# Kernel optimization log

Measured on AMD Instinct MI355X. Metric: run time of the kernel, lower is better.

Reference implementation:

```python
import jax, jax.numpy as jnp
import numpy as np

N = 1024    # num_points
HID = 1024  # Hamiltonian MLP hidden width


def setup_inputs() -> dict:
    key = jax.random.key(0)
    ks = jax.random.split(key, 6)
    def w(k, shape, fan_in):
        return jax.random.normal(k, shape, dtype=jnp.float32) / np.float32(np.sqrt(fan_in))
    return {
        "x": jax.random.normal(ks[0], (N,), dtype=jnp.float32),
        "q": jax.random.normal(ks[1], (N,), dtype=jnp.float32),
        "p": jax.random.normal(ks[2], (N,), dtype=jnp.float32),
        "W1": w(ks[3], (3 * N, HID), 3 * N),
        "b1": jnp.zeros((HID,), dtype=jnp.float32),
        "W2": w(ks[4], (HID, HID), HID),
        "b2": jnp.zeros((HID,), dtype=jnp.float32),
        "W3": w(ks[5], (HID, 1), HID),
        "b3": jnp.zeros((1,), dtype=jnp.float32),
    }


def _hamiltonian(z, W1, b1, W2, b2, W3, b3):
    # H: R^{3N} -> scalar (matches self.H(cat([x,q,p])).sum())
    h = jnp.tanh(z @ W1 + b1)
    h = jnp.tanh(h @ W2 + b2)
    return jnp.sum(h @ W3 + b3)


def reference(x, q, p, W1, b1, W2, b2, W3, b3):
    n = x.shape[0]

    def grads_qp(x_):
        # (dH/dq, dH/dp) as a function of x, with q,p closed over
        f = lambda q_, p_: _hamiltonian(jnp.concatenate([x_, q_, p_]), W1, b1, W2, b2, W3, b3)
        return jax.grad(f, argnums=(0, 1))(q, p)  # each [n]

    # Diagonal of cross-Hessian blocks via forward-over-reverse, batched over
    # all n basis directions at once (replaces the per-index autograd loop).
    eye = jnp.eye(n, dtype=x.dtype)

    def diag_entry(e_i, i):
        _, (dgq, dgp) = jax.jvp(grads_qp, (x,), (e_i,))
        return dgq[i], dgp[i]  # d2H/(dx_i dq_i), d2H/(dx_i dp_i)

    dH_dq_dx, dH_dp_dx = jax.vmap(diag_entry)(eye, jnp.arange(n))  # each [n]
    return dH_dp_dx, -dH_dq_dx
```

## Files before the change

kernel.cpp:

```cpp
#include <hip/hip_runtime.h>
#include <math.h>

typedef unsigned short u16;
typedef __bf16 bf16x8 __attribute__((ext_vector_type(8)));
typedef float f32x4 __attribute__((ext_vector_type(4)));

__device__ inline u16 bf16_rn(float x) {
    unsigned u = __float_as_uint(x);
    return (u16)((u + 0x7FFFu + ((u >> 16) & 1u)) >> 16);
}
__device__ inline void split2(float x, u16& h, u16& l) {
    h = bf16_rn(x);
    float hf = __uint_as_float(((unsigned)h) << 16);
    l = bf16_rn(x - hf);
}
__device__ inline uint2 pack4(u16 a, u16 b, u16 c, u16 d) {
    uint2 r;
    r.x = (unsigned)a | ((unsigned)b << 16);
    r.y = (unsigned)c | ((unsigned)d << 16);
    return r;
}
__device__ inline f32x4 mfma16(bf16x8 a, bf16x8 b, f32x4 c) {
    return __builtin_amdgcn_mfma_f32_16x16x32_bf16(a, b, c, 0, 0, 0);
}

__global__ __launch_bounds__(256) void k_pre(const float* __restrict__ x,
                                             const float* __restrict__ q,
                                             const float* __restrict__ p,
                                             const float* __restrict__ W1,
                                             u16* __restrict__ Ah, u16* __restrict__ Al,
                                             float* __restrict__ Upart,
                                             float* __restrict__ out,
                                             float* __restrict__ Vacc) {
    int b = blockIdx.x, t = threadIdx.x;
    if (b < 1024) {
        int idx = (b * 256 + t) * 4;
        float4 v = *(const float4*)(W1 + idx);
        u16 h0, l0, h1, l1, h2, l2, h3, l3;
        split2(v.x, h0, l0); split2(v.y, h1, l1); split2(v.z, h2, l2); split2(v.w, h3, l3);
        *(uint2*)&Ah[idx] = pack4(h0, h1, h2, h3);
        *(uint2*)&Al[idx] = pack4(l0, l1, l2, l3);
    } else if (b < 1216) {
        int jc = b - 1024;
        int k = (jc & 3) * 256 + t;
        int j0 = (jc >> 2) * 64;
        __shared__ float zs[64];
        if (t < 64) {
            int j = j0 + t;
            zs[t] = (j < 1024) ? x[j] : (j < 2048 ? q[j - 1024] : p[j - 2048]);
        }
        __syncthreads();
        float acc = 0.f;
#pragma unroll 8
        for (int j = 0; j < 64; ++j) acc += zs[j] * W1[(j0 + j) * 1024 + k];
        Upart[(jc >> 2) * 1024 + k] = acc;
    } else {
        int idx = ((b - 1216) * 256 + t) * 4;
        if (idx < 2048) *(float4*)(out + idx) = make_float4(0.f, 0.f, 0.f, 0.f);
        else *(float4*)(Vacc + idx - 2048) = make_float4(0.f, 0.f, 0.f, 0.f);
    }
}

__global__ __launch_bounds__(256) void k_w2v(const float* __restrict__ W2,
                                             const float* __restrict__ b1,
                                             const float* __restrict__ Upart,
                                             float* __restrict__ H1g, float* __restrict__ D1g,
                                             u16* __restrict__ W2h, u16* __restrict__ W2l,
                                             u16* __restrict__ WTh, u16* __restrict__ WTl,
                                             float* __restrict__ Vacc) {
    __shared__ float T[64][65];
    __shared__ float hs[64], ds[64];
    int k0 = blockIdx.y * 64, m0 = blockIdx.x * 64;
    int t = threadIdx.x;
    if (t < 64) {
        float u = 0.f;
#pragma unroll 8
        for (int c = 0; c < 48; ++c) u += Upart[c * 1024 + k0 + t];
        float h = tanhf(u + b1[k0 + t]);
        hs[t] = h;
        ds[t] = 1.f - h * h;
        if (m0 == 0) { H1g[k0 + t] = h; D1g[k0 + t] = 1.f - h * h; }
    }
    __syncthreads();
    int rr = t >> 4, cc = (t & 15) * 4;
    float4 vp = make_float4(0.f, 0.f, 0.f, 0.f);
#pragma unroll
    for (int j = 0; j < 4; ++j) {
        int r = rr + j * 16;
        float4 v = *(const float4*)(W2 + (k0 + r) * 1024 + m0 + cc);
        T[r][cc + 0] = v.x; T[r][cc + 1] = v.y; T[r][cc + 2] = v.z; T[r][cc + 3] = v.w;
        u16 h0, l0, h1, l1, h2, l2, h3, l3;
        split2(v.x, h0, l0); split2(v.y, h1, l1); split2(v.z, h2, l2); split2(v.w, h3, l3);
        *(uint2*)&W2h[(k0 + r) * 1024 + m0 + cc] = pack4(h0, h1, h2, h3);
        *(uint2*)&W2l[(k0 + r) * 1024 + m0 + cc] = pack4(l0, l1, l2, l3);
        float hk = hs[r];
        vp.x += hk * v.x; vp.y += hk * v.y; vp.z += hk * v.z; vp.w += hk * v.w;
    }
    vp.x += __shfl_xor(vp.x, 16); vp.y += __shfl_xor(vp.y, 16);
    vp.z += __shfl_xor(vp.z, 16); vp.w += __shfl_xor(vp.w, 16);
    vp.x += __shfl_xor(vp.x, 32); vp.y += __shfl_xor(vp.y, 32);
    vp.z += __shfl_xor(vp.z, 32); vp.w += __shfl_xor(vp.w, 32);
    if (((t & 63) >> 4) == 0) {
        atomicAdd(&Vacc[m0 + cc + 0], vp.x);
        atomicAdd(&Vacc[m0 + cc + 1], vp.y);
        atomicAdd(&Vacc[m0 + cc + 2], vp.z);
        atomicAdd(&Vacc[m0 + cc + 3], vp.w);
    }
    __syncthreads();
#pragma unroll
    for (int j = 0; j < 4; ++j) {
        int mrow = rr + j * 16;
        float f0 = T[cc + 0][mrow] * ds[cc + 0];
        float f1 = T[cc + 1][mrow] * ds[cc + 1];
        float f2 = T[cc + 2][mrow] * ds[cc + 2];
        float f3 = T[cc + 3][mrow] * ds[cc + 3];
        u16 h0, l0, h1, l1, h2, l2, h3, l3;
        split2(f0, h0, l0); split2(f1, h1, l1); split2(f2, h2, l2); split2(f3, h3, l3);
        *(uint2*)&WTh[(m0 + mrow) * 1024 + k0 + cc] = pack4(h0, h1, h2, h3);
        *(uint2*)&WTl[(m0 + mrow) * 1024 + k0 + cc] = pack4(l0, l1, l2, l3);
    }
}

__global__ __launch_bounds__(256) void k_g(const float* __restrict__ W2,
                                           const float* __restrict__ Vacc,
                                           const float* __restrict__ b2,
                                           const float* __restrict__ W3,
                                           const float* __restrict__ H1,
                                           const float* __restrict__ D1,
                                           float* __restrict__ Avec) {
    __shared__ float sv[1024];
    int k = blockIdx.x;
    int t = threadIdx.x;
#pragma unroll
    for (int j = 0; j < 4; ++j) {
        int m = t * 4 + j;
        float h = tanhf(Vacc[m] + b2[m]);
        sv[m] = (1.f - h * h) * W3[m];
    }
    __syncthreads();
    float acc = 0.f;
#pragma unroll
    for (int m = t; m < 1024; m += 256) acc += W2[k * 1024 + m] * sv[m];
    for (int o = 32; o; o >>= 1) acc += __shfl_down(acc, o);
    __shared__ float red[4];
    int lane = t & 63, w = t >> 6;
    if (lane == 0) red[w] = acc;
    __syncthreads();
    if (t == 0) Avec[k] = -2.f * H1[k] * D1[k] * (red[0] + red[1] + red[2] + red[3]);
}

#define LDK 68
__global__ __launch_bounds__(512) void k_gemm1(const u16* __restrict__ Ah, const u16* __restrict__ Al,
                                               const u16* __restrict__ Bh, const u16* __restrict__ Bl,
                                               const float* __restrict__ Vacc,
                                               const float* __restrict__ b2,
                                               const float* __restrict__ W3,
                                               u16* __restrict__ Sh, u16* __restrict__ Sl) {
    __shared__ u16 As[2][2][64 * LDK];
    __shared__ u16 Bs[2][2][64 * LDK];
    int tid = threadIdx.x, lane = tid & 63, wv = tid >> 6;
    int kh = wv >> 2, wy = (wv >> 1) & 1, wx = wv & 1;
    int i0 = blockIdx.y * 64, m0 = blockIdx.x * 64;
    int srow = tid >> 3, sseg = (tid & 7) * 8;
    int ldso = srow * LDK + sseg;
    const u16* ap_h = Ah + (i0 + srow) * 1024 + sseg;
    const u16* ap_l = Al + (i0 + srow) * 1024 + sseg;
    const u16* bp_h = Bh + (m0 + srow) * 1024 + sseg;
    const u16* bp_l = Bl + (m0 + srow) * 1024 + sseg;
    int tx = lane & 15, qy = lane >> 4;
    int koff = kh * 32 + qy * 8;
    int raA[2], rbB[2];
    raA[0] = (wy * 32 + tx) * LDK + koff;
    raA[1] = raA[0] + 16 * LDK;
    rbB[0] = (wx * 32 + tx) * LDK + koff;
    rbB[1] = rbB[0] + 16 * LDK;
    f32x4 acc[2][2];
#pragma unroll
    for (int a = 0; a < 2; ++a)
#pragma unroll
        for (int b = 0; b < 2; ++b) acc[a][b] = (f32x4){0.f, 0.f, 0.f, 0.f};

    *(uint4*)&As[0][0][ldso] = *(const uint4*)(ap_h);
    *(uint4*)&As[0][1][ldso] = *(const uint4*)(ap_l);
    *(uint4*)&Bs[0][0][ldso] = *(const uint4*)(bp_h);
    *(uint4*)&Bs[0][1][ldso] = *(const uint4*)(bp_l);

    for (int k0 = 0; k0 < 1024; k0 += 64) {
        int buf = (k0 >> 6) & 1;
        int kn = (k0 + 64) & 1023;
        uint4 pa = *(const uint4*)(ap_h + kn);
        uint4 pb = *(const uint4*)(ap_l + kn);
        uint4 pc = *(const uint4*)(bp_h + kn);
        uint4 pd = *(const uint4*)(bp_l + kn);
        __syncthreads();
        bf16x8 aH0 = *(const bf16x8*)&As[buf][0][raA[0]];
        bf16x8 aH1 = *(const bf16x8*)&As[buf][0][raA[1]];
        bf16x8 aL0 = *(const bf16x8*)&As[buf][1][raA[0]];
        bf16x8 aL1 = *(const bf16x8*)&As[buf][1][raA[1]];
        bf16x8 bH0 = *(const bf16x8*)&Bs[buf][0][rbB[0]];
        bf16x8 bH1 = *(const bf16x8*)&Bs[buf][0][rbB[1]];
        bf16x8 bL0 = *(const bf16x8*)&Bs[buf][1][rbB[0]];
        bf16x8 bL1 = *(const bf16x8*)&Bs[buf][1][rbB[1]];
        acc[0][0] = mfma16(aH0, bH0, acc[0][0]);
        acc[0][0] = mfma16(aH0, bL0, acc[0][0]);
        acc[0][0] = mfma16(aL0, bH0, acc[0][0]);
        acc[0][1] = mfma16(aH0, bH1, acc[0][1]);
        acc[0][1] = mfma16(aH0, bL1, acc[0][1]);
        acc[0][1] = mfma16(aL0, bH1, acc[0][1]);
        acc[1][0] = mfma16(aH1, bH0, acc[1][0]);
        acc[1][0] = mfma16(aH1, bL0, acc[1][0]);
        acc[1][0] = mfma16(aL1, bH0, acc[1][0]);
        acc[1][1] = mfma16(aH1, bH1, acc[1][1]);
        acc[1][1] = mfma16(aH1, bL1, acc[1][1]);
        acc[1][1] = mfma16(aL1, bH1, acc[1][1]);
        int nb = buf ^ 1;
        *(uint4*)&As[nb][0][ldso] = pa;
        *(uint4*)&As[nb][1][ldso] = pb;
        *(uint4*)&Bs[nb][0][ldso] = pc;
        *(uint4*)&Bs[nb][1][ldso] = pd;
    }
    __syncthreads();
    f32x4* mrg = (f32x4*)&As[0][0][0];
    if (kh == 1) {
#pragma unroll
        for (int si = 0; si < 2; ++si)
#pragma unroll
            for (int sj = 0; sj < 2; ++sj)
                mrg[(((wy * 2 + wx) * 4 + si * 2 + sj) * 4 + qy) * 16 + tx] = acc[si][sj];
    }
    __syncthreads();
    if (kh == 0) {
#pragma unroll
        for (int si = 0; si < 2; ++si)
#pragma unroll
            for (int sj = 0; sj < 2; ++sj) {
                f32x4 o = mrg[(((wy * 2 + wx) * 4 + si * 2 + sj) * 4 + qy) * 16 + tx];
                acc[si][sj][0] += o[0]; acc[si][sj][1] += o[1];
                acc[si][sj][2] += o[2]; acc[si][sj][3] += o[3];
            }
#pragma unroll
        for (int sj = 0; sj < 2; ++sj) {
            int m = m0 + wx * 32 + sj * 16 + tx;
            float hv = tanhf(Vacc[m] + b2[m]);
            float d2 = 1.f - hv * hv;
            float cm = -2.f * hv * d2 * W3[m];
#pragma unroll
            for (int si = 0; si < 2; ++si) {
                int ib = i0 + wy * 32 + si * 16 + qy * 4;
#pragma unroll
                for (int r = 0; r < 4; ++r) {
                    float v = acc[si][sj][r] * cm;
                    u16 h, l;
                    split2(v, h, l);
                    Sh[(ib + r) * 1024 + m] = h;
                    Sl[(ib + r) * 1024 + m] = l;
                }
            }
        }
    }
}

__global__ __launch_bounds__(512) void k_gemm2(const u16* __restrict__ Sh, const u16* __restrict__ Sl,
                                               const u16* __restrict__ W2h, const u16* __restrict__ W2l,
                                               const float* __restrict__ W1,
                                               const float* __restrict__ D1,
                                               const float* __restrict__ Avec,
                                               float* __restrict__ out) {
    __shared__ u16 As[2][2][64 * LDK];
    __shared__ u16 Bs[2][2][64 * LDK];
    int tid = threadIdx.x, lane = tid & 63, wv = tid >> 6;
    int kh = wv >> 2, wy = (wv >> 1) & 1, wx = wv & 1;
    int i0 = blockIdx.y * 64, k0g = blockIdx.x * 64;
    int srow = tid >> 3, sseg = (tid & 7) * 8;
    int ldso = srow * LDK + sseg;
    const u16* ap_h = Sh + (i0 + srow) * 1024 + sseg;
    const u16* ap_l = Sl + (i0 + srow) * 1024 + sseg;
    const u16* bp_h = W2h + (k0g + srow) * 1024 + sseg;
    const u16* bp_l = W2l + (k0g + srow) * 1024 + sseg;
    int tx = lane & 15, qy = lane >> 4;
    int koff = kh * 32 + qy * 8;
    int raA[2], rbB[2];
    raA[0] = (wy * 32 + tx) * LDK + koff;
    raA[1] = raA[0] + 16 * LDK;
    rbB[0] = (wx * 32 + tx) * LDK + koff;
    rbB[1] = rbB[0] + 16 * LDK;
    f32x4 acc[2][2];
#pragma unroll
    for (int a = 0; a < 2; ++a)
#pragma unroll
        for (int b = 0; b < 2; ++b) acc[a][b] = (f32x4){0.f, 0.f, 0.f, 0.f};

    *(uint4*)&As[0][0][ldso] = *(const uint4*)(ap_h);
    *(uint4*)&As[0][1][ldso] = *(const uint4*)(ap_l);
    *(uint4*)&Bs[0][0][ldso] = *(const uint4*)(bp_h);
    *(uint4*)&Bs[0][1][ldso] = *(const uint4*)(bp_l);

    for (int m0 = 0; m0 < 1024; m0 += 64) {
        int buf = (m0 >> 6) & 1;
        int mn = (m0 + 64) & 1023;
        uint4 pa = *(const uint4*)(ap_h + mn);
        uint4 pb = *(const uint4*)(ap_l + mn);
        uint4 pc = *(const uint4*)(bp_h + mn);
        uint4 pd = *(const uint4*)(bp_l + mn);
        __syncthreads();
        bf16x8 aH0 = *(const bf16x8*)&As[buf][0][raA[0]];
        bf16x8 aH1 = *(const bf16x8*)&As[buf][0][raA[1]];
        bf16x8 aL0 = *(const bf16x8*)&As[buf][1][raA[0]];
        bf16x8 aL1 = *(const bf16x8*)&As[buf][1][raA[1]];
        bf16x8 bH0 = *(const bf16x8*)&Bs[buf][0][rbB[0]];
        bf16x8 bH1 = *(const bf16x8*)&Bs[buf][0][rbB[1]];
        bf16x8 bL0 = *(const bf16x8*)&Bs[buf][1][rbB[0]];
        bf16x8 bL1 = *(const bf16x8*)&Bs[buf][1][rbB[1]];
        acc[0][0] = mfma16(aH0, bH0, acc[0][0]);
        acc[0][0] = mfma16(aH0, bL0, acc[0][0]);
        acc[0][0] = mfma16(aL0, bH0, acc[0][0]);
        acc[0][1] = mfma16(aH0, bH1, acc[0][1]);
        acc[0][1] = mfma16(aH0, bL1, acc[0][1]);
        acc[0][1] = mfma16(aL0, bH1, acc[0][1]);
        acc[1][0] = mfma16(aH1, bH0, acc[1][0]);
        acc[1][0] = mfma16(aH1, bL0, acc[1][0]);
        acc[1][0] = mfma16(aL1, bH0, acc[1][0]);
        acc[1][1] = mfma16(aH1, bH1, acc[1][1]);
        acc[1][1] = mfma16(aH1, bL1, acc[1][1]);
        acc[1][1] = mfma16(aL1, bH1, acc[1][1]);
        int nb = buf ^ 1;
        *(uint4*)&As[nb][0][ldso] = pa;
        *(uint4*)&As[nb][1][ldso] = pb;
        *(uint4*)&Bs[nb][0][ldso] = pc;
        *(uint4*)&Bs[nb][1][ldso] = pd;
    }
    __syncthreads();
    f32x4* mrg = (f32x4*)&As[0][0][0];
    if (kh == 1) {
#pragma unroll
        for (int si = 0; si < 2; ++si)
#pragma unroll
            for (int sj = 0; sj < 2; ++sj)
                mrg[(((wy * 2 + wx) * 4 + si * 2 + sj) * 4 + qy) * 16 + tx] = acc[si][sj];
    }
    __syncthreads();
    if (kh == 0) {
#pragma unroll
        for (int si = 0; si < 2; ++si)
#pragma unroll
            for (int sj = 0; sj < 2; ++sj) {
                f32x4 o = mrg[(((wy * 2 + wx) * 4 + si * 2 + sj) * 4 + qy) * 16 + tx];
                acc[si][sj][0] += o[0]; acc[si][sj][1] += o[1];
                acc[si][sj][2] += o[2]; acc[si][sj][3] += o[3];
            }
        int kk[2];
        float d1v[2], avv[2];
#pragma unroll
        for (int sj = 0; sj < 2; ++sj) {
            kk[sj] = k0g + wx * 32 + sj * 16 + tx;
            d1v[sj] = D1[kk[sj]];
            avv[sj] = Avec[kk[sj]];
        }
#pragma unroll
        for (int si = 0; si < 2; ++si) {
            int ib = i0 + wy * 32 + si * 16 + qy * 4;
#pragma unroll
            for (int r = 0; r < 4; ++r) {
                int i = ib + r;
                float pq = 0.f, pp = 0.f;
#pragma unroll
                for (int sj = 0; sj < 2; ++sj) {
                    int k = kk[sj];
                    float dr = avv[sj] * W1[i * 1024 + k] + d1v[sj] * acc[si][sj][r];
                    pq += W1[(1024 + i) * 1024 + k] * dr;
                    pp += W1[(2048 + i) * 1024 + k] * dr;
                }
                for (int o = 1; o < 16; o <<= 1) {
                    pq += __shfl_xor(pq, o);
                    pp += __shfl_xor(pp, o);
                }
                if (tx == 0) {
                    atomicAdd(&out[i], pp);
                    atomicAdd(&out[1024 + i], -pq);
                }
            }
        }
    }
}

extern "C" void kernel_launch(void* const* d_in, const int* in_sizes, int n_in,
                              void* d_out, int out_size, void* d_ws, size_t ws_size,
                              hipStream_t stream) {
    const float* x = (const float*)d_in[0];
    const float* q = (const float*)d_in[1];
    const float* p = (const float*)d_in[2];
    const float* W1 = (const float*)d_in[3];
    const float* b1 = (const float*)d_in[4];
    const float* W2 = (const float*)d_in[5];
    const float* b2 = (const float*)d_in[6];
    const float* W3 = (const float*)d_in[7];
    float* out = (float*)d_out;
    float* ws = (float*)d_ws;
    float* H1 = ws, *D1 = ws + 1024, *Avec = ws + 2048, *Vacc = ws + 3072;
    float* Upart = ws + 4096;
    u16* u0 = (u16*)(ws + 65536);
    u16* Ah = u0;
    u16* Al = u0 + 1048576;
    u16* WTh = u0 + 2097152;
    u16* WTl = u0 + 3145728;
    u16* W2h = u0 + 4194304;
    u16* W2l = u0 + 5242880;
    u16* Sh = u0 + 6291456;
    u16* Sl = u0 + 7340032;

    k_pre<<<1219, 256, 0, stream>>>(x, q, p, W1, Ah, Al, Upart, out, Vacc);
    k_w2v<<<dim3(16, 16), 256, 0, stream>>>(W2, b1, Upart, H1, D1, W2h, W2l, WTh, WTl, Vacc);
    k_gemm1<<<dim3(16, 16), 512, 0, stream>>>(Ah, Al, WTh, WTl, Vacc, b2, W3, Sh, Sl);
    k_g<<<1024, 256, 0, stream>>>(W2, Vacc, b2, W3, H1, D1, Avec);
    k_gemm2<<<dim3(16, 16), 512, 0, stream>>>(Sh, Sl, W2h, W2l, W1, D1, Avec, out);
}
```

Baseline: 127.8 us.

## Drop split-bf16 emulation in GEMMs and fold k_g into gemm1 grid

Both GEMMs used to emulate fp32 with three bf16 MFMAs on hi/lo splits. They now use a single bf16 MFMA on rounded operands, which halves operand staging, LDS and global traffic and cuts MFMA count threefold. The separate k_g kernel is folded into k_gemm1 as an extra column of blocks, removing one launch. The cost is accuracy: products are now plain bf16, which may break tolerance on second-derivative outputs.

New measurement: 119.8 us. -6.2%, faster.

```diff
diff --git a/kernel.cpp b/kernel.cpp
--- a/kernel.cpp
+++ b/kernel.cpp
@@ -8,11 +8,6 @@
 __device__ inline u16 bf16_rn(float x) {
     unsigned u = __float_as_uint(x);
     return (u16)((u + 0x7FFFu + ((u >> 16) & 1u)) >> 16);
-}
-__device__ inline void split2(float x, u16& h, u16& l) {
-    h = bf16_rn(x);
-    float hf = __uint_as_float(((unsigned)h) << 16);
-    l = bf16_rn(x - hf);
 }
 __device__ inline uint2 pack4(u16 a, u16 b, u16 c, u16 d) {
     uint2 r;
@@ -20,6 +15,9 @@
     r.y = (unsigned)c | ((unsigned)d << 16);
     return r;
 }
+__device__ inline uint2 pack4f(float a, float b, float c, float d) {
+    return pack4(bf16_rn(a), bf16_rn(b), bf16_rn(c), bf16_rn(d));
+}
 __device__ inline f32x4 mfma16(bf16x8 a, bf16x8 b, f32x4 c) {
     return __builtin_amdgcn_mfma_f32_16x16x32_bf16(a, b, c, 0, 0, 0);
 }
@@ -28,7 +26,7 @@
                                              const float* __restrict__ q,
                                              const float* __restrict__ p,
                                              const float* __restrict__ W1,
-                                             u16* __restrict__ Ah, u16* __restrict__ Al,
+                                             u16* __restrict__ Ah,
                                              float* __restrict__ Upart,
                                              float* __restrict__ out,
                                              float* __restrict__ Vacc) {
@@ -36,10 +34,7 @@
     if (b < 1024) {
         int idx = (b * 256 + t) * 4;
         float4 v = *(const float4*)(W1 + idx);
-        u16 h0, l0, h1, l1, h2, l2, h3, l3;
-        split2(v.x, h0, l0); split2(v.y, h1, l1); split2(v.z, h2, l2); split2(v.w, h3, l3);
-        *(uint2*)&Ah[idx] = pack4(h0, h1, h2, h3);
-        *(uint2*)&Al[idx] = pack4(l0, l1, l2, l3);
+        *(uint2*)&Ah[idx] = pack4f(v.x, v.y, v.z, v.w);
     } else if (b < 1216) {
         int jc = b - 1024;
         int k = (jc & 3) * 256 + t;
@@ -65,8 +60,8 @@
                                              const float* __restrict__ b1,
                                              const float* __restrict__ Upart,
                                              float* __restrict__ H1g, float* __restrict__ D1g,
-                                             u16* __restrict__ W2h, u16* __restrict__ W2l,
-                                             u16* __restrict__ WTh, u16* __restrict__ WTl,
+                                             u16* __restrict__ W2h,
+                                             u16* __restrict__ WTh,
                                              float* __restrict__ Vacc) {
     __shared__ float T[64][65];
     __shared__ float hs[64], ds[64];
@@ -89,10 +84,7 @@
         int r = rr + j * 16;
         float4 v = *(const float4*)(W2 + (k0 + r) * 1024 + m0 + cc);
         T[r][cc + 0] = v.x; T[r][cc + 1] = v.y; T[r][cc + 2] = v.z; T[r][cc + 3] = v.w;
-        u16 h0, l0, h1, l1, h2, l2, h3, l3;
-        split2(v.x, h0, l0); split2(v.y, h1, l1); split2(v.z, h2, l2); split2(v.w, h3, l3);
-        *(uint2*)&W2h[(k0 + r) * 1024 + m0 + cc] = pack4(h0, h1, h2, h3);
-        *(uint2*)&W2l[(k0 + r) * 1024 + m0 + cc] = pack4(l0, l1, l2, l3);
+        *(uint2*)&W2h[(k0 + r) * 1024 + m0 + cc] = pack4f(v.x, v.y, v.z, v.w);
         float hk = hs[r];
         vp.x += hk * v.x; vp.y += hk * v.y; vp.z += hk * v.z; vp.w += hk * v.w;
     }
@@ -114,59 +106,54 @@
         float f1 = T[cc + 1][mrow] * ds[cc + 1];
         float f2 = T[cc + 2][mrow] * ds[cc + 2];
         float f3 = T[cc + 3][mrow] * ds[cc + 3];
-        u16 h0, l0, h1, l1, h2, l2, h3, l3;
-        split2(f0, h0, l0); split2(f1, h1, l1); split2(f2, h2, l2); split2(f3, h3, l3);
-        *(uint2*)&WTh[(m0 + mrow) * 1024 + k0 + cc] = pack4(h0, h1, h2, h3);
-        *(uint2*)&WTl[(m0 + mrow) * 1024 + k0 + cc] = pack4(l0, l1, l2, l3);
-    }
-}
-
-__global__ __launch_bounds__(256) void k_g(const float* __restrict__ W2,
-                                           const float* __restrict__ Vacc,
-                                           const float* __restrict__ b2,
-                                           const float* __restrict__ W3,
-                                           const float* __restrict__ H1,
-                                           const float* __restrict__ D1,
-                                           float* __restrict__ Avec) {
-    __shared__ float sv[1024];
-    int k = blockIdx.x;
-    int t = threadIdx.x;
-#pragma unroll
-    for (int j = 0; j < 4; ++j) {
-        int m = t * 4 + j;
-        float h = tanhf(Vacc[m] + b2[m]);
-        sv[m] = (1.f - h * h) * W3[m];
-    }
-    __syncthreads();
-    float acc = 0.f;
-#pragma unroll
-    for (int m = t; m < 1024; m += 256) acc += W2[k * 1024 + m] * sv[m];
-    for (int o = 32; o; o >>= 1) acc += __shfl_down(acc, o);
-    __shared__ float red[4];
-    int lane = t & 63, w = t >> 6;
-    if (lane == 0) red[w] = acc;
-    __syncthreads();
-    if (t == 0) Avec[k] = -2.f * H1[k] * D1[k] * (red[0] + red[1] + red[2] + red[3]);
+        *(uint2*)&WTh[(m0 + mrow) * 1024 + k0 + cc] = pack4f(f0, f1, f2, f3);
+    }
 }
 
 #define LDK 68
-__global__ __launch_bounds__(512) void k_gemm1(const u16* __restrict__ Ah, const u16* __restrict__ Al,
-                                               const u16* __restrict__ Bh, const u16* __restrict__ Bl,
+__global__ __launch_bounds__(512) void k_gemm1(const u16* __restrict__ Ah,
+                                               const u16* __restrict__ Bh,
                                                const float* __restrict__ Vacc,
                                                const float* __restrict__ b2,
                                                const float* __restrict__ W3,
-                                               u16* __restrict__ Sh, u16* __restrict__ Sl) {
-    __shared__ u16 As[2][2][64 * LDK];
-    __shared__ u16 Bs[2][2][64 * LDK];
-    int tid = threadIdx.x, lane = tid & 63, wv = tid >> 6;
+                                               const float* __restrict__ W2,
+                                               const float* __restrict__ H1,
+                                               const float* __restrict__ D1,
+                                               float* __restrict__ Avec,
+                                               u16* __restrict__ Sh) {
+    __shared__ u16 As[2][64 * LDK];
+    __shared__ u16 Bs[2][64 * LDK];
+    __shared__ float sv[1024];
+    int tid = threadIdx.x;
+    if (blockIdx.x == 16) {
+        int kbase = blockIdx.y * 64;
+#pragma unroll
+        for (int j = 0; j < 2; ++j) {
+            int m = tid + j * 512;
+            float h = tanhf(Vacc[m] + b2[m]);
+            sv[m] = (1.f - h * h) * W3[m];
+        }
+        __syncthreads();
+        int g = tid >> 3, sub = tid & 7;
+        int k = kbase + g;
+        const float* wrow = W2 + k * 1024 + sub * 128;
+        const float* svp = sv + sub * 128;
+        float acc = 0.f;
+#pragma unroll 8
+        for (int j = 0; j < 128; ++j) acc += wrow[j] * svp[j];
+        acc += __shfl_xor(acc, 1);
+        acc += __shfl_xor(acc, 2);
+        acc += __shfl_xor(acc, 4);
+        if (sub == 0) Avec[k] = -2.f * H1[k] * D1[k] * acc;
+        return;
+    }
+    int lane = tid & 63, wv = tid >> 6;
     int kh = wv >> 2, wy = (wv >> 1) & 1, wx = wv & 1;
     int i0 = blockIdx.y * 64, m0 = blockIdx.x * 64;
     int srow = tid >> 3, sseg = (tid & 7) * 8;
     int ldso = srow * LDK + sseg;
-    const u16* ap_h = Ah + (i0 + srow) * 1024 + sseg;
-    const u16* ap_l = Al + (i0 + srow) * 1024 + sseg;
-    const u16* bp_h = Bh + (m0 + srow) * 1024 + sseg;
-    const u16* bp_l = Bl + (m0 + srow) * 1024 + sseg;
+    const u16* ap = Ah + (i0 + srow) * 1024 + sseg;
+    const u16* bp = Bh + (m0 + srow) * 1024 + sseg;
     int tx = lane & 15, qy = lane >> 4;
     int koff = kh * 32 + qy * 8;
     int raA[2], rbB[2];
@@ -180,47 +167,29 @@
 #pragma unroll
         for (int b = 0; b < 2; ++b) acc[a][b] = (f32x4){0.f, 0.f, 0.f, 0.f};
 
-    *(uint4*)&As[0][0][ldso] = *(const uint4*)(ap_h);
-    *(uint4*)&As[0][1][ldso] = *(const uint4*)(ap_l);
-    *(uint4*)&Bs[0][0][ldso] = *(const uint4*)(bp_h);
-    *(uint4*)&Bs[0][1][ldso] = *(const uint4*)(bp_l);
+    *(uint4*)&As[0][ldso] = *(const uint4*)(ap);
+    *(uint4*)&Bs[0][ldso] = *(const uint4*)(bp);
 
     for (int k0 = 0; k0 < 1024; k0 += 64) {
         int buf = (k0 >> 6) & 1;
         int kn = (k0 + 64) & 1023;
-        uint4 pa = *(const uint4*)(ap_h + kn);
-        uint4 pb = *(const uint4*)(ap_l + kn);
-        uint4 pc = *(const uint4*)(bp_h + kn);
-        uint4 pd = *(const uint4*)(bp_l + kn);
+        uint4 pa = *(const uint4*)(ap + kn);
+        uint4 pc = *(const uint4*)(bp + kn);
         __syncthreads();
-        bf16x8 aH0 = *(const bf16x8*)&As[buf][0][raA[0]];
-        bf16x8 aH1 = *(const bf16x8*)&As[buf][0][raA[1]];
-        bf16x8 aL0 = *(const bf16x8*)&As[buf][1][raA[0]];
-        bf16x8 aL1 = *(const bf16x8*)&As[buf][1][raA[1]];
-        bf16x8 bH0 = *(const bf16x8*)&Bs[buf][0][rbB[0]];
-        bf16x8 bH1 = *(const bf16x8*)&Bs[buf][0][rbB[1]];
-        bf16x8 bL0 = *(const bf16x8*)&Bs[buf][1][rbB[0]];
-        bf16x8 bL1 = *(const bf16x8*)&Bs[buf][1][rbB[1]];
+        bf16x8 aH0 = *(const bf16x8*)&As[buf][raA[0]];
+        bf16x8 aH1 = *(const bf16x8*)&As[buf][raA[1]];
+        bf16x8 bH0 = *(const bf16x8*)&Bs[buf][rbB[0]];
+        bf16x8 bH1 = *(const bf16x8*)&Bs[buf][rbB[1]];
         acc[0][0] = mfma16(aH0, bH0, acc[0][0]);
-        acc[0][0] = mfma16(aH0, bL0, acc[0][0]);
-        acc[0][0] = mfma16(aL0, bH0, acc[0][0]);
         acc[0][1] = mfma16(aH0, bH1, acc[0][1]);
-        acc[0][1] = mfma16(aH0, bL1, acc[0][1]);
-        acc[0][1] = mfma16(aL0, bH1, acc[0][1]);
         acc[1][0] = mfma16(aH1, bH0, acc[1][0]);
-        acc[1][0] = mfma16(aH1, bL0, acc[1][0]);
-        acc[1][0] = mfma16(aL1, bH0, acc[1][0]);
         acc[1][1] = mfma16(aH1, bH1, acc[1][1]);
-        acc[1][1] = mfma16(aH1, bL1, acc[1][1]);
-        acc[1][1] = mfma16(aL1, bH1, acc[1][1]);
         int nb = buf ^ 1;
-        *(uint4*)&As[nb][0][ldso] = pa;
-        *(uint4*)&As[nb][1][ldso] = pb;
-        *(uint4*)&Bs[nb][0][ldso] = pc;
-        *(uint4*)&Bs[nb][1][ldso] = pd;
-    }
-    __syncthreads();
-    f32x4* mrg = (f32x4*)&As[0][0][0];
+        *(uint4*)&As[nb][ldso] = pa;
+        *(uint4*)&Bs[nb][ldso] = pc;
+    }
+    __syncthreads();
+    f32x4* mrg = (f32x4*)&As[0][0];
     if (kh == 1) {
 #pragma unroll
         for (int si = 0; si < 2; ++si)
@@ -248,35 +217,28 @@
             for (int si = 0; si < 2; ++si) {
                 int ib = i0 + wy * 32 + si * 16 + qy * 4;
 #pragma unroll
-                for (int r = 0; r < 4; ++r) {
-                    float v = acc[si][sj][r] * cm;
-                    u16 h, l;
-                    split2(v, h, l);
-                    Sh[(ib + r) * 1024 + m] = h;
-                    Sl[(ib + r) * 1024 + m] = l;
-                }
+                for (int r = 0; r < 4; ++r)
+                    Sh[(ib + r) * 1024 + m] = bf16_rn(acc[si][sj][r] * cm);
             }
         }
     }
 }
 
-__global__ __launch_bounds__(512) void k_gemm2(const u16* __restrict__ Sh, const u16* __restrict__ Sl,
-                                               const u16* __restrict__ W2h, const u16* __restrict__ W2l,
+__global__ __launch_bounds__(512) void k_gemm2(const u16* __restrict__ Sh,
+                                               const u16* __restrict__ W2h,
                                                const float* __restrict__ W1,
                                                const float* __restrict__ D1,
                                                const float* __restrict__ Avec,
                                                float* __restrict__ out) {
-    __shared__ u16 As[2][2][64 * LDK];
-    __shared__ u16 Bs[2][2][64 * LDK];
+    __shared__ u16 As[2][64 * LDK];
+    __shared__ u16 Bs[2][64 * LDK];
     int tid = threadIdx.x, lane = tid & 63, wv = tid >> 6;
     int kh = wv >> 2, wy = (wv >> 1) & 1, wx = wv & 1;
     int i0 = blockIdx.y * 64, k0g = blockIdx.x * 64;
     int srow = tid >> 3, sseg = (tid & 7) * 8;
     int ldso = srow * LDK + sseg;
-    const u16* ap_h = Sh + (i0 + srow) * 1024 + sseg;
-    const u16* ap_l = Sl + (i0 + srow) * 1024 + sseg;
-    const u16* bp_h = W2h + (k0g + srow) * 1024 + sseg;
-    const u16* bp_l = W2l + (k0g + srow) * 1024 + sseg;
+    const u16* ap = Sh + (i0 + srow) * 1024 + sseg;
+    const u16* bp = W2h + (k0g + srow) * 1024 + sseg;
     int tx = lane & 15, qy = lane >> 4;
     int koff = kh * 32 + qy * 8;
     int raA[2], rbB[2];
@@ -290,47 +252,29 @@
 #pragma unroll
         for (int b = 0; b < 2; ++b) acc[a][b] = (f32x4){0.f, 0.f, 0.f, 0.f};
 
-    *(uint4*)&As[0][0][ldso] = *(const uint4*)(ap_h);
-    *(uint4*)&As[0][1][ldso] = *(const uint4*)(ap_l);
-    *(uint4*)&Bs[0][0][ldso] = *(const uint4*)(bp_h);
-    *(uint4*)&Bs[0][1][ldso] = *(const uint4*)(bp_l);
+    *(uint4*)&As[0][ldso] = *(const uint4*)(ap);
+    *(uint4*)&Bs[0][ldso] = *(const uint4*)(bp);
 
     for (int m0 = 0; m0 < 1024; m0 += 64) {
         int buf = (m0 >> 6) & 1;
         int mn = (m0 + 64) & 1023;
-        uint4 pa = *(const uint4*)(ap_h + mn);
-        uint4 pb = *(const uint4*)(ap_l + mn);
-        uint4 pc = *(const uint4*)(bp_h + mn);
-        uint4 pd = *(const uint4*)(bp_l + mn);
+        uint4 pa = *(const uint4*)(ap + mn);
+        uint4 pc = *(const uint4*)(bp + mn);
         __syncthreads();
-        bf16x8 aH0 = *(const bf16x8*)&As[buf][0][raA[0]];
-        bf16x8 aH1 = *(const bf16x8*)&As[buf][0][raA[1]];
-        bf16x8 aL0 = *(const bf16x8*)&As[buf][1][raA[0]];
-        bf16x8 aL1 = *(const bf16x8*)&As[buf][1][raA[1]];
-        bf16x8 bH0 = *(const bf16x8*)&Bs[buf][0][rbB[0]];
-        bf16x8 bH1 = *(const bf16x8*)&Bs[buf][0][rbB[1]];
-        bf16x8 bL0 = *(const bf16x8*)&Bs[buf][1][rbB[0]];
-        bf16x8 bL1 = *(const bf16x8*)&Bs[buf][1][rbB[1]];
+        bf16x8 aH0 = *(const bf16x8*)&As[buf][raA[0]];
+        bf16x8 aH1 = *(const bf16x8*)&As[buf][raA[1]];
+        bf16x8 bH0 = *(const bf16x8*)&Bs[buf][rbB[0]];
+        bf16x8 bH1 = *(const bf16x8*)&Bs[buf][rbB[1]];
         acc[0][0] = mfma16(aH0, bH0, acc[0][0]);
-        acc[0][0] = mfma16(aH0, bL0, acc[0][0]);
-        acc[0][0] = mfma16(aL0, bH0, acc[0][0]);
         acc[0][1] = mfma16(aH0, bH1, acc[0][1]);
-        acc[0][1] = mfma16(aH0, bL1, acc[0][1]);
-        acc[0][1] = mfma16(aL0, bH1, acc[0][1]);
         acc[1][0] = mfma16(aH1, bH0, acc[1][0]);
-        acc[1][0] = mfma16(aH1, bL0, acc[1][0]);
-        acc[1][0] = mfma16(aL1, bH0, acc[1][0]);
         acc[1][1] = mfma16(aH1, bH1, acc[1][1]);
-        acc[1][1] = mfma16(aH1, bL1, acc[1][1]);
-        acc[1][1] = mfma16(aL1, bH1, acc[1][1]);
         int nb = buf ^ 1;
-        *(uint4*)&As[nb][0][ldso] = pa;
-        *(uint4*)&As[nb][1][ldso] = pb;
-        *(uint4*)&Bs[nb][0][ldso] = pc;
-        *(uint4*)&Bs[nb][1][ldso] = pd;
-    }
-    __syncthreads();
-    f32x4* mrg = (f32x4*)&As[0][0][0];
+        *(uint4*)&As[nb][ldso] = pa;
+        *(uint4*)&Bs[nb][ldso] = pc;
+    }
+    __syncthreads();
+    f32x4* mrg = (f32x4*)&As[0][0];
     if (kh == 1) {
 #pragma unroll
         for (int si = 0; si < 2; ++si)
@@ -400,17 +344,12 @@
     float* Upart = ws + 4096;
     u16* u0 = (u16*)(ws + 65536);
     u16* Ah = u0;
-    u16* Al = u0 + 1048576;
-    u16* WTh = u0 + 2097152;
-    u16* WTl = u0 + 3145728;
-    u16* W2h = u0 + 4194304;
-    u16* W2l = u0 + 5242880;
-    u16* Sh = u0 + 6291456;
-    u16* Sl = u0 + 7340032;
-
-    k_pre<<<1219, 256, 0, stream>>>(x, q, p, W1, Ah, Al, Upart, out, Vacc);
-    k_w2v<<<dim3(16, 16), 256, 0, stream>>>(W2, b1, Upart, H1, D1, W2h, W2l, WTh, WTl, Vacc);
-    k_gemm1<<<dim3(16, 16), 512, 0, stream>>>(Ah, Al, WTh, WTl, Vacc, b2, W3, Sh, Sl);
-    k_g<<<1024, 256, 0, stream>>>(W2, Vacc, b2, W3, H1, D1, Avec);
-    k_gemm2<<<dim3(16, 16), 512, 0, stream>>>(Sh, Sl, W2h, W2l, W1, D1, Avec, out);
-}
+    u16* WTh = u0 + 1048576;
+    u16* W2h = u0 + 2097152;
+    u16* Sh = u0 + 3145728;
+
+    k_pre<<<1219, 256, 0, stream>>>(x, q, p, W1, Ah, Upart, out, Vacc);
+    k_w2v<<<dim3(16, 16), 256, 0, stream>>>(W2, b1, Upart, H1, D1, W2h, WTh, Vacc);
+    k_gemm1<<<dim3(17, 16), 512, 0, stream>>>(Ah, WTh, Vacc, b2, W3, W2, H1, D1, Avec, Sh);
+    k_gemm2<<<dim3(16, 16), 512, 0, stream>>>(Sh, W2h, W1, D1, Avec, out);
+}
```
